# Kernel optimization log

Measured on AMD Instinct MI355X. Metric: run time of the kernel, lower is better.

## Reference

```python
import jax, jax.numpy as jnp
import numpy as np

B, S, D_MODEL, H = 2, 2048, 1024, 16
HD = D_MODEL // H  # head_dim = 64


def _rope_sincos(seq_len, dim, dtype=jnp.float32):
    # inv_freq = 1 / 10000**(arange(0, dim, 2)/dim)
    inv_freq = 1.0 / (10000.0 ** (jnp.arange(0, dim, 2, dtype=dtype) / dim))
    ang = jnp.arange(seq_len, dtype=dtype)[:, None] * inv_freq[None, :]  # [S, dim/2]
    # reshape for broadcast over the head axis of [B, S, H, dim]
    return jnp.sin(ang)[:, None, :], jnp.cos(ang)[:, None, :]  # [S,1,dim/2]


def _apply_rope(x, sin, cos):
    # x: [B, S, H, HD]; interleaved even/odd rotation, matching
    # stack([x1*cos - x2*sin, x1*sin + x2*cos], -1).flatten(-2,-1)
    x1, x2 = x[..., 0::2], x[..., 1::2]
    rot = jnp.stack([x1 * cos - x2 * sin, x1 * sin + x2 * cos], axis=-1)
    return rot.reshape(x.shape)


def setup_inputs() -> dict:
    key = jax.random.key(0)
    ks = jax.random.split(key, 9)
    std = 0.02
    inp = {
        "hidden_states": jax.random.normal(ks[0], (B, S, D_MODEL), jnp.float32),
        "attention_mask": jnp.zeros((1, 1, S, S), jnp.float32),
        "Wq": jax.random.normal(ks[1], (D_MODEL, D_MODEL), jnp.float32) * std,
        "bq": jnp.zeros((D_MODEL,), jnp.float32),
        "Wk": jax.random.normal(ks[2], (D_MODEL, D_MODEL), jnp.float32) * std,
        "bk": jnp.zeros((D_MODEL,), jnp.float32),
        "Wv": jax.random.normal(ks[3], (D_MODEL, D_MODEL), jnp.float32) * std,
        "bv": jnp.zeros((D_MODEL,), jnp.float32),
        "Wo": jax.random.normal(ks[4], (D_MODEL, D_MODEL), jnp.float32) * std,
        "bo": jnp.zeros((D_MODEL,), jnp.float32),
    }
    return inp


def reference(hidden_states, attention_mask, Wq, bq, Wk, bk, Wv, bv, Wo, bo):
    b, s, d = hidden_states.shape
    # QKV projections -> [B, S, H, HD]
    q = (hidden_states @ Wq + bq).reshape(b, s, H, HD)
    k = (hidden_states @ Wk + bk).reshape(b, s, H, HD)
    v = (hidden_states @ Wv + bv).reshape(b, s, H, HD)

    sin, cos = _rope_sincos(s, HD, hidden_states.dtype)
    q = _apply_rope(q, sin, cos)
    k = _apply_rope(k, sin, cos)

    scale = 1.0 / jnp.sqrt(jnp.asarray(HD, hidden_states.dtype))
    # [B, H, S, S]
    scores = jnp.einsum("bqhd,bkhd->bhqk", q, k) * scale + attention_mask
    probs = jax.nn.softmax(scores, axis=-1)
    # [B, S, H, HD] -> [B, S, D]
    ctx = jnp.einsum("bhqk,bkhd->bqhd", probs, v).reshape(b, s, d)
    return ctx @ Wo + bo
```

## Files before the change

kernel.cpp:

```cpp
#include <hip/hip_runtime.h>
#include <hip/hip_bf16.h>

typedef unsigned short u16;
typedef __attribute__((ext_vector_type(8))) __bf16 bf16x8;
typedef __attribute__((ext_vector_type(4))) float f32x4;
typedef __attribute__((ext_vector_type(16))) float f32x16;
typedef __attribute__((ext_vector_type(4))) unsigned uint4v;

#define AS1 __attribute__((address_space(1)))
#define AS3 __attribute__((address_space(3)))

#define S_LEN 2048
#define NH 16
#define DM 1024
#define BATCH 2

__device__ __forceinline__ u16 f2b(float f) {
  union { float f; unsigned u; } v; v.f = f;
  unsigned r = v.u + 0x7FFFu + ((v.u >> 16) & 1u);
  return (u16)(r >> 16);
}

__device__ __forceinline__ unsigned pk2(float lo, float hi) {
  __bf16 l = (__bf16)lo, h = (__bf16)hi;
  unsigned short ul = __builtin_bit_cast(unsigned short, l);
  unsigned short uh = __builtin_bit_cast(unsigned short, h);
  return (unsigned)ul | ((unsigned)uh << 16);
}

__device__ __forceinline__ float exp2_raw(float x) {
  float r;
  asm("v_exp_f32 %0, %1" : "=v"(r) : "v"(x));
  return r;
}

__global__ void rope_table_kernel(float2* __restrict__ t) {
  int idx = blockIdx.x * 256 + threadIdx.x;
  if (idx < S_LEN * 32) {
    int s = idx >> 5, i = idx & 31;
    float inv = powf(10000.f, -(float)i * (1.f / 32.f));
    float ang = (float)s * inv;
    t[idx] = make_float2(sinf(ang), cosf(ang));
  }
}

__global__ void cvt_bf16_kernel(const float* __restrict__ x, u16* __restrict__ y) {
  int i = (blockIdx.x * 256 + threadIdx.x) * 4;
  float4 v = *(const float4*)(x + i);
  *(ushort4*)(y + i) = make_ushort4(f2b(v.x), f2b(v.y), f2b(v.z), f2b(v.w));
}

__global__ void transpose_all_kernel(const float* __restrict__ Wq, const float* __restrict__ Wk,
                                     const float* __restrict__ Wv, const float* __restrict__ Wo,
                                     u16* __restrict__ out) {
  __shared__ float tile[32][33];
  const int z = blockIdx.z;
  const float* W = z == 0 ? Wq : z == 1 ? Wk : z == 2 ? Wv : Wo;
  u16* Wt = out + (size_t)z * DM * DM;
  const int bx = blockIdx.x * 32;
  const int by = blockIdx.y * 32;
  const int tx = threadIdx.x, ty = threadIdx.y;
  for (int i = ty; i < 32; i += 8)
    tile[i][tx] = W[(size_t)(by + i) * DM + bx + tx];
  __syncthreads();
  for (int i = ty; i < 32; i += 8)
    Wt[(size_t)(bx + i) * DM + by + tx] = f2b(tile[tx][i]);
}

template <int MODE>
__global__ __launch_bounds__(256) void gemm128(const u16* __restrict__ A,
                                               const u16* __restrict__ Bt,
                                               const float* __restrict__ bias0,
                                               const float* __restrict__ bias1,
                                               const float* __restrict__ bias2,
                                               void* __restrict__ out0,
                                               void* __restrict__ out1,
                                               void* __restrict__ out2,
                                               const float2* __restrict__ sc,
                                               float escale) {
  __shared__ u16 Al[128 * 32];
  __shared__ u16 Bl[128 * 32];
  const int t = threadIdx.x;
  const int lane = t & 63;
  const int wid = t >> 6;
  const int wr = wid >> 1, wc = wid & 1;
  const int row0 = blockIdx.x * 128, col0 = blockIdx.y * 128;

  const int arow = t >> 2, acol = (t & 3) * 8;
  const u16* gA0 = A + (size_t)(row0 + arow) * DM + acol;
  const u16* gA1 = gA0 + (size_t)64 * DM;
  const u16* gB0 = Bt + (size_t)(col0 + arow) * DM + acol;
  const u16* gB1 = gB0 + (size_t)64 * DM;

  f32x4 acc[4][4] = {};

  for (int k0 = 0; k0 < DM; k0 += 32) {
    __builtin_amdgcn_global_load_lds((const AS1 void*)(gA0 + k0), (AS3 void*)(&Al[t * 8]), 16, 0, 0);
    __builtin_amdgcn_global_load_lds((const AS1 void*)(gA1 + k0), (AS3 void*)(&Al[2048 + t * 8]), 16, 0, 0);
    __builtin_amdgcn_global_load_lds((const AS1 void*)(gB0 + k0), (AS3 void*)(&Bl[t * 8]), 16, 0, 0);
    __builtin_amdgcn_global_load_lds((const AS1 void*)(gB1 + k0), (AS3 void*)(&Bl[2048 + t * 8]), 16, 0, 0);
    __syncthreads();
    bf16x8 af[4], bfr[4];
#pragma unroll
    for (int m = 0; m < 4; ++m)
      af[m] = *(const bf16x8*)&Al[(wr * 64 + m * 16 + (lane & 15)) * 32 + (lane >> 4) * 8];
#pragma unroll
    for (int n = 0; n < 4; ++n)
      bfr[n] = *(const bf16x8*)&Bl[(wc * 64 + n * 16 + (lane & 15)) * 32 + (lane >> 4) * 8];
#pragma unroll
    for (int m = 0; m < 4; ++m)
#pragma unroll
      for (int n = 0; n < 4; ++n)
        acc[m][n] = __builtin_amdgcn_mfma_f32_16x16x32_bf16(af[m], bfr[n], acc[m][n], 0, 0, 0);
    __syncthreads();
  }

  const int sec = (MODE == 3) ? (col0 >> 10) : 0;
  const float* bias = (MODE == 3) ? (sec == 0 ? bias0 : sec == 1 ? bias1 : bias2) : bias0;
  const float es = (MODE == 3 && sec != 0) ? 1.f : escale;

#pragma unroll
  for (int m = 0; m < 4; ++m) {
#pragma unroll
    for (int n = 0; n < 4; ++n) {
      const int col = col0 + wc * 64 + n * 16 + (lane & 15);
      const float bcol = bias[col & 1023];
      const int rbase = row0 + wr * 64 + m * 16 + ((lane >> 4) << 2);
      if constexpr (MODE == 3) {
        const int colr = col & 1023;
        const int h = colr >> 6, d = colr & 63;
        if (sec < 2) {
          u16* O = (u16*)(sec == 0 ? out0 : out1);
          const int ip = d >> 1;
#pragma unroll
          for (int r = 0; r < 4; ++r) {
            const int row = rbase + r;
            const int bb = row >> 11, ss = row & (S_LEN - 1);
            float v = acc[m][n][r] + bcol;
            float pr = __shfl_xor(v, 1, 64);
            float2 scv = sc[ss * 32 + ip];
            float o = (d & 1) ? fmaf(pr, scv.x, v * scv.y) : fmaf(-pr, scv.x, v * scv.y);
            O[((size_t)(bb * NH + h) * S_LEN + ss) * 64 + d] = f2b(o * es);
          }
        } else {
          u16* O = (u16*)out2;
#pragma unroll
          for (int r = 0; r < 4; ++r) {
            const int row = rbase + r;
            const int bb = row >> 11, ss = row & (S_LEN - 1);
            O[((size_t)(bb * NH + h) * 64 + d) * S_LEN + ss] = f2b(acc[m][n][r] + bcol);
          }
        }
      } else {
        float* O = (float*)out0;
#pragma unroll
        for (int r = 0; r < 4; ++r) {
          const int row = rbase + r;
          O[(size_t)row * DM + col] = acc[m][n][r] + bcol;
        }
      }
    }
  }
}

__global__ __launch_bounds__(256, 2) void attn64(const u16* __restrict__ Qa,
                                                 const u16* __restrict__ Ka,
                                                 const u16* __restrict__ Vt,
                                                 u16* __restrict__ Ctx) {
  __shared__ u16 Kl[2][8192];
  __shared__ u16 Vl[2][8192];
  const int t = threadIdx.x, lane = t & 63, w = t >> 6;
  const int l31 = lane & 31, hi = lane >> 5;

  const int wg = blockIdx.x;
  const int swz = (wg & 7) * 64 + (wg >> 3);
  const int bh = swz >> 4, qb = swz & 15;
  const int bb = bh / NH, h = bh % NH;
  const u16* Q = Qa + (size_t)bh * S_LEN * 64;
  const u16* K = Ka + (size_t)bh * S_LEN * 64;
  const u16* V = Vt + (size_t)bh * 64 * S_LEN;
  const int qr0 = qb * 128 + w * 32;

  bf16x8 bQ[4];
#pragma unroll
  for (int kc = 0; kc < 4; ++kc)
    bQ[kc] = *(const bf16x8*)&Q[(size_t)(qr0 + l31) * 64 + kc * 16 + hi * 8];

  int off0[4];
#pragma unroll
  for (int kc = 0; kc < 4; ++kc) {
    const int cb = kc * 32 + hi * 16;
    off0[kc] = l31 * 128 + (cb ^ ((l31 & 7) << 4));
  }

  float mrun = -3.0e38f, lrun = 0.f;
  f32x16 acco0 = {}, acco1 = {};

#define STAGE64(kv, c, hf)                                                               \
  {                                                                                      \
    _Pragma("unroll") for (int is = 0; is < 2; ++is) {                                   \
      const int o = is * 4096 + t * 16;                                                  \
      const int row = o >> 7;                                                            \
      const int cs = (o & 127) ^ ((row & 7) << 4);                                       \
      __builtin_amdgcn_global_load_lds((const AS1 void*)(K + (size_t)((kv) + row) * 64 + (cs >> 1)), \
                                       (AS3 void*)(&Kl[c][(hf) * 4096 + (o >> 1)]), 16, 0, 0); \
      __builtin_amdgcn_global_load_lds((const AS1 void*)(V + (size_t)row * S_LEN + (kv) + (cs >> 1)), \
                                       (AS3 void*)(&Vl[c][(hf) * 4096 + (o >> 1)]), 16, 0, 0); \
    }                                                                                    \
  }
#define STAGE128(kv, c) { STAGE64((kv), c, 0); STAGE64((kv) + 64, c, 1); }

  STAGE128(0, 0);
  __syncthreads();
  int cur = 0;

  for (int it = 0; it < S_LEN / 128; ++it) {
    if (it + 1 < S_LEN / 128) STAGE128((it + 1) * 128, cur ^ 1);

#pragma unroll
    for (int hf = 0; hf < 2; ++hf) {
      const char* KC = (const char*)Kl[cur] + hf * 8192;
      const char* VC = (const char*)Vl[cur] + hf * 8192;

      f32x16 s0 = {}, s1 = {};
      __builtin_amdgcn_s_setprio(1);
#pragma unroll
      for (int kc = 0; kc < 4; ++kc) {
        bf16x8 aK0 = *(const bf16x8*)(KC + off0[kc]);
        bf16x8 aK1 = *(const bf16x8*)(KC + off0[kc] + 4096);
        s0 = __builtin_amdgcn_mfma_f32_32x32x16_bf16(aK0, bQ[kc], s0, 0, 0, 0);
        s1 = __builtin_amdgcn_mfma_f32_32x32x16_bf16(aK1, bQ[kc], s1, 0, 0, 0);
      }
      __builtin_amdgcn_s_setprio(0);

      float p[32];
#pragma unroll
      for (int i = 0; i < 16; ++i) { p[i] = s0[i]; p[16 + i] = s1[i]; }

      float mm[10];
#pragma unroll
      for (int i = 0; i < 10; ++i)
        mm[i] = fmaxf(fmaxf(p[3 * i], p[3 * i + 1]), p[3 * i + 2]);
      const float n0 = fmaxf(fmaxf(mm[0], mm[1]), mm[2]);
      const float n1 = fmaxf(fmaxf(mm[3], mm[4]), mm[5]);
      const float n2 = fmaxf(fmaxf(mm[6], mm[7]), mm[8]);
      const float n3 = fmaxf(mm[9], fmaxf(p[30], p[31]));
      float pmax = fmaxf(fmaxf(n0, n1), fmaxf(n2, n3));
      pmax = fmaxf(pmax, __shfl_xor(pmax, 32, 64));

      if (!__all(pmax - mrun <= 8.f)) {
        const float mnew = fmaxf(mrun, pmax);
        const float al = exp2_raw(mrun - mnew);
#pragma unroll
        for (int i = 0; i < 16; ++i) { acco0[i] *= al; acco1[i] *= al; }
        lrun *= al;
        mrun = mnew;
      }
#pragma unroll
      for (int i = 0; i < 32; ++i) p[i] = exp2_raw(p[i] - mrun);

      float b16[16];
#pragma unroll
      for (int i = 0; i < 16; ++i) b16[i] = p[i] + p[16 + i];
      float b8[8];
#pragma unroll
      for (int i = 0; i < 8; ++i) b8[i] = b16[i] + b16[8 + i];
      float b4[4];
#pragma unroll
      for (int i = 0; i < 4; ++i) b4[i] = b8[i] + b8[4 + i];
      float rs = (b4[0] + b4[1]) + (b4[2] + b4[3]);
      rs += __shfl_xor(rs, 32, 64);
      lrun += rs;

#pragma unroll
      for (int ch = 0; ch < 4; ++ch) {
        const int base = (ch >> 1) * 16 + (ch & 1) * 8;
        unsigned a0 = pk2(p[base + 0], p[base + 1]);
        unsigned b0 = pk2(p[base + 2], p[base + 3]);
        unsigned a8 = pk2(p[base + 4], p[base + 5]);
        unsigned b8w = pk2(p[base + 6], p[base + 7]);
        asm("v_permlane32_swap_b32 %0, %1" : "+v"(a0), "+v"(a8));
        asm("v_permlane32_swap_b32 %0, %1" : "+v"(b0), "+v"(b8w));
        uint4v bw;
        bw[0] = a0; bw[1] = b0; bw[2] = a8; bw[3] = b8w;
        const bf16x8 bP = __builtin_bit_cast(bf16x8, bw);
        bf16x8 aV0 = *(const bf16x8*)(VC + off0[ch]);
        bf16x8 aV1 = *(const bf16x8*)(VC + off0[ch] + 4096);
        __builtin_amdgcn_s_setprio(1);
        acco0 = __builtin_amdgcn_mfma_f32_32x32x16_bf16(aV0, bP, acco0, 0, 0, 0);
        acco1 = __builtin_amdgcn_mfma_f32_32x32x16_bf16(aV1, bP, acco1, 0, 0, 0);
        __builtin_amdgcn_s_setprio(0);
      }
    }

    __syncthreads();
    cur ^= 1;
  }

  const float inv = 1.f / lrun;
  const size_t rowbase = ((size_t)bb * S_LEN + qr0 + l31) * DM + h * 64;
#pragma unroll
  for (int u = 0; u < 4; ++u) {
    ushort4 o0, o1;
    o0.x = f2b(acco0[4 * u + 0] * inv); o0.y = f2b(acco0[4 * u + 1] * inv);
    o0.z = f2b(acco0[4 * u + 2] * inv); o0.w = f2b(acco0[4 * u + 3] * inv);
    o1.x = f2b(acco1[4 * u + 0] * inv); o1.y = f2b(acco1[4 * u + 1] * inv);
    o1.z = f2b(acco1[4 * u + 2] * inv); o1.w = f2b(acco1[4 * u + 3] * inv);
    *(ushort4*)&Ctx[rowbase + 8 * u + 4 * hi] = o0;
    *(ushort4*)&Ctx[rowbase + 32 + 8 * u + 4 * hi] = o1;
  }
}

extern "C" void kernel_launch(void* const* d_in, const int* in_sizes, int n_in,
                              void* d_out, int out_size, void* d_ws, size_t ws_size,
                              hipStream_t stream) {
  const float* hs = (const float*)d_in[0];
  const float* Wq = (const float*)d_in[2];
  const float* bq = (const float*)d_in[3];
  const float* Wk = (const float*)d_in[4];
  const float* bk = (const float*)d_in[5];
  const float* Wv = (const float*)d_in[6];
  const float* bv = (const float*)d_in[7];
  const float* Wo = (const float*)d_in[8];
  const float* bo = (const float*)d_in[9];

  u16* Xbf = (u16*)d_ws;
  u16* Wt4 = Xbf + (size_t)4096 * 1024;
  u16* Qa  = Wt4 + (size_t)4096 * 1024;
  u16* Ka  = Qa + (size_t)4096 * 1024;
  u16* Vtb = Ka + (size_t)4096 * 1024;
  u16* Ctx = Vtb + (size_t)4096 * 1024;
  float2* scT = (float2*)(Ctx + (size_t)4096 * 1024);

  const float SC = 0.125f * 1.44269504088896f;

  rope_table_kernel<<<dim3(256), dim3(256), 0, stream>>>(scT);
  cvt_bf16_kernel<<<dim3(4096), dim3(256), 0, stream>>>(hs, Xbf);
  transpose_all_kernel<<<dim3(32, 32, 4), dim3(32, 8), 0, stream>>>(Wq, Wk, Wv, Wo, Wt4);

  gemm128<3><<<dim3(32, 24), dim3(256), 0, stream>>>(Xbf, Wt4, bq, bk, bv,
                                                     (void*)Qa, (void*)Ka, (void*)Vtb, scT, SC);

  attn64<<<dim3(512), dim3(256), 0, stream>>>(Qa, Ka, Vtb, Ctx);

  gemm128<2><<<dim3(32, 8), dim3(256), 0, stream>>>(Ctx, Wt4 + (size_t)3 * DM * DM, bo,
                                                    nullptr, nullptr, d_out, nullptr, nullptr,
                                                    nullptr, 1.f);
}
```

Before: 147.3 us.

## Split attention KV across waves, merge prep kernels, narrow output GEMM tiles

Three preprocessing kernels are merged into one launch to cut launch overhead. The attention kernel now processes 64 query rows per block with two wave pairs each covering half of the key/value sequence, combining partial softmax states through LDS at the end. It drops double-buffered prefetch in favour of higher occupancy (4 blocks/SM) and twice the blocks. The output projection uses 128x64 tiles to double its grid for better CU fill, at the cost of more A-matrix reloads.

New measurement: 139.3 us. 1.06x faster.

```diff
diff --git a/kernel.cpp b/kernel.cpp
--- a/kernel.cpp
+++ b/kernel.cpp
@@ -34,50 +34,51 @@
   return r;
 }
 
-__global__ void rope_table_kernel(float2* __restrict__ t) {
-  int idx = blockIdx.x * 256 + threadIdx.x;
-  if (idx < S_LEN * 32) {
-    int s = idx >> 5, i = idx & 31;
+__global__ __launch_bounds__(256) void prep_kernel(const float* __restrict__ hs,
+                                                   const float* __restrict__ Wq,
+                                                   const float* __restrict__ Wk,
+                                                   const float* __restrict__ Wv,
+                                                   const float* __restrict__ Wo,
+                                                   u16* __restrict__ Xbf,
+                                                   u16* __restrict__ Wt4,
+                                                   float2* __restrict__ scT) {
+  __shared__ float tile[32][33];
+  const int bid = blockIdx.x, t = threadIdx.x;
+  if (bid < 4096) {
+    const int i = (bid * 256 + t) * 4;
+    float4 v = *(const float4*)(hs + i);
+    *(ushort4*)(Xbf + i) = make_ushort4(f2b(v.x), f2b(v.y), f2b(v.z), f2b(v.w));
+  } else if (bid < 8192) {
+    const int zb = bid - 4096;
+    const int z = zb >> 10, rem = zb & 1023;
+    const int bx = (rem & 31) * 32, by = (rem >> 5) * 32;
+    const float* W = z == 0 ? Wq : z == 1 ? Wk : z == 2 ? Wv : Wo;
+    u16* Wt = Wt4 + (size_t)z * DM * DM;
+    const int tx = t & 31, ty = t >> 5;
+    for (int i = ty; i < 32; i += 8)
+      tile[i][tx] = W[(size_t)(by + i) * DM + bx + tx];
+    __syncthreads();
+    for (int i = ty; i < 32; i += 8)
+      Wt[(size_t)(bx + i) * DM + by + tx] = f2b(tile[tx][i]);
+  } else {
+    const int idx = (bid - 8192) * 256 + t;
+    const int s = idx >> 5, i = idx & 31;
     float inv = powf(10000.f, -(float)i * (1.f / 32.f));
     float ang = (float)s * inv;
-    t[idx] = make_float2(sinf(ang), cosf(ang));
-  }
-}
-
-__global__ void cvt_bf16_kernel(const float* __restrict__ x, u16* __restrict__ y) {
-  int i = (blockIdx.x * 256 + threadIdx.x) * 4;
-  float4 v = *(const float4*)(x + i);
-  *(ushort4*)(y + i) = make_ushort4(f2b(v.x), f2b(v.y), f2b(v.z), f2b(v.w));
-}
-
-__global__ void transpose_all_kernel(const float* __restrict__ Wq, const float* __restrict__ Wk,
-                                     const float* __restrict__ Wv, const float* __restrict__ Wo,
-                                     u16* __restrict__ out) {
-  __shared__ float tile[32][33];
-  const int z = blockIdx.z;
-  const float* W = z == 0 ? Wq : z == 1 ? Wk : z == 2 ? Wv : Wo;
-  u16* Wt = out + (size_t)z * DM * DM;
-  const int bx = blockIdx.x * 32;
-  const int by = blockIdx.y * 32;
-  const int tx = threadIdx.x, ty = threadIdx.y;
-  for (int i = ty; i < 32; i += 8)
-    tile[i][tx] = W[(size_t)(by + i) * DM + bx + tx];
-  __syncthreads();
-  for (int i = ty; i < 32; i += 8)
-    Wt[(size_t)(bx + i) * DM + by + tx] = f2b(tile[tx][i]);
-}
-
-template <int MODE>
-__global__ __launch_bounds__(256) void gemm128(const u16* __restrict__ A,
-                                               const u16* __restrict__ Bt,
-                                               const float* __restrict__ bias0,
-                                               const float* __restrict__ bias1,
-                                               const float* __restrict__ bias2,
-                                               void* __restrict__ out0,
-                                               void* __restrict__ out1,
-                                               void* __restrict__ out2,
-                                               const float2* __restrict__ sc,
-                                               float escale) {
+    scT[idx] = make_float2(sinf(ang), cosf(ang));
+  }
+}
+
+__global__ __launch_bounds__(256) void gemm_qkv(const u16* __restrict__ A,
+                                                const u16* __restrict__ Bt,
+                                                const float* __restrict__ bias0,
+                                                const float* __restrict__ bias1,
+                                                const float* __restrict__ bias2,
+                                                u16* __restrict__ out0,
+                                                u16* __restrict__ out1,
+                                                u16* __restrict__ out2,
+                                                const float2* __restrict__ sc,
+                                                float escale) {
   __shared__ u16 Al[128 * 32];
   __shared__ u16 Bl[128 * 32];
   const int t = threadIdx.x;
@@ -115,9 +116,9 @@
     __syncthreads();
   }
 
-  const int sec = (MODE == 3) ? (col0 >> 10) : 0;
-  const float* bias = (MODE == 3) ? (sec == 0 ? bias0 : sec == 1 ? bias1 : bias2) : bias0;
-  const float es = (MODE == 3 && sec != 0) ? 1.f : escale;
+  const int sec = col0 >> 10;
+  const float* bias = sec == 0 ? bias0 : sec == 1 ? bias1 : bias2;
+  const float es = sec == 0 ? escale : 1.f;
 
 #pragma unroll
   for (int m = 0; m < 4; ++m) {
@@ -126,60 +127,106 @@
       const int col = col0 + wc * 64 + n * 16 + (lane & 15);
       const float bcol = bias[col & 1023];
       const int rbase = row0 + wr * 64 + m * 16 + ((lane >> 4) << 2);
-      if constexpr (MODE == 3) {
-        const int colr = col & 1023;
-        const int h = colr >> 6, d = colr & 63;
-        if (sec < 2) {
-          u16* O = (u16*)(sec == 0 ? out0 : out1);
-          const int ip = d >> 1;
-#pragma unroll
-          for (int r = 0; r < 4; ++r) {
-            const int row = rbase + r;
-            const int bb = row >> 11, ss = row & (S_LEN - 1);
-            float v = acc[m][n][r] + bcol;
-            float pr = __shfl_xor(v, 1, 64);
-            float2 scv = sc[ss * 32 + ip];
-            float o = (d & 1) ? fmaf(pr, scv.x, v * scv.y) : fmaf(-pr, scv.x, v * scv.y);
-            O[((size_t)(bb * NH + h) * S_LEN + ss) * 64 + d] = f2b(o * es);
-          }
-        } else {
-          u16* O = (u16*)out2;
-#pragma unroll
-          for (int r = 0; r < 4; ++r) {
-            const int row = rbase + r;
-            const int bb = row >> 11, ss = row & (S_LEN - 1);
-            O[((size_t)(bb * NH + h) * 64 + d) * S_LEN + ss] = f2b(acc[m][n][r] + bcol);
-          }
+      const int colr = col & 1023;
+      const int h = colr >> 6, d = colr & 63;
+      if (sec < 2) {
+        u16* O = sec == 0 ? out0 : out1;
+        const int ip = d >> 1;
+#pragma unroll
+        for (int r = 0; r < 4; ++r) {
+          const int row = rbase + r;
+          const int bb = row >> 11, ss = row & (S_LEN - 1);
+          float v = acc[m][n][r] + bcol;
+          float pr = __shfl_xor(v, 1, 64);
+          float2 scv = sc[ss * 32 + ip];
+          float o = (d & 1) ? fmaf(pr, scv.x, v * scv.y) : fmaf(-pr, scv.x, v * scv.y);
+          O[((size_t)(bb * NH + h) * S_LEN + ss) * 64 + d] = f2b(o * es);
         }
       } else {
-        float* O = (float*)out0;
+        u16* O = out2;
 #pragma unroll
         for (int r = 0; r < 4; ++r) {
           const int row = rbase + r;
-          O[(size_t)row * DM + col] = acc[m][n][r] + bcol;
+          const int bb = row >> 11, ss = row & (S_LEN - 1);
+          O[((size_t)(bb * NH + h) * 64 + d) * S_LEN + ss] = f2b(acc[m][n][r] + bcol);
         }
       }
     }
   }
 }
 
-__global__ __launch_bounds__(256, 2) void attn64(const u16* __restrict__ Qa,
+__global__ __launch_bounds__(256) void gemm_o(const u16* __restrict__ A,
+                                              const u16* __restrict__ Bt,
+                                              const float* __restrict__ bias,
+                                              float* __restrict__ O) {
+  __shared__ u16 Al[128 * 32];
+  __shared__ u16 Bl[64 * 32];
+  const int t = threadIdx.x;
+  const int lane = t & 63;
+  const int wid = t >> 6;
+  const int wr = wid >> 1, wc = wid & 1;
+  const int row0 = blockIdx.x * 128, col0 = blockIdx.y * 64;
+
+  const int arow = t >> 2, acol = (t & 3) * 8;
+  const u16* gA0 = A + (size_t)(row0 + arow) * DM + acol;
+  const u16* gA1 = gA0 + (size_t)64 * DM;
+  const u16* gB0 = Bt + (size_t)(col0 + arow) * DM + acol;
+
+  f32x4 acc[4][2] = {};
+
+  for (int k0 = 0; k0 < DM; k0 += 32) {
+    __builtin_amdgcn_global_load_lds((const AS1 void*)(gA0 + k0), (AS3 void*)(&Al[t * 8]), 16, 0, 0);
+    __builtin_amdgcn_global_load_lds((const AS1 void*)(gA1 + k0), (AS3 void*)(&Al[2048 + t * 8]), 16, 0, 0);
+    __builtin_amdgcn_global_load_lds((const AS1 void*)(gB0 + k0), (AS3 void*)(&Bl[t * 8]), 16, 0, 0);
+    __syncthreads();
+    bf16x8 af[4], bfr[2];
+#pragma unroll
+    for (int m = 0; m < 4; ++m)
+      af[m] = *(const bf16x8*)&Al[(wr * 64 + m * 16 + (lane & 15)) * 32 + (lane >> 4) * 8];
+#pragma unroll
+    for (int n = 0; n < 2; ++n)
+      bfr[n] = *(const bf16x8*)&Bl[(wc * 32 + n * 16 + (lane & 15)) * 32 + (lane >> 4) * 8];
+#pragma unroll
+    for (int m = 0; m < 4; ++m)
+#pragma unroll
+      for (int n = 0; n < 2; ++n)
+        acc[m][n] = __builtin_amdgcn_mfma_f32_16x16x32_bf16(af[m], bfr[n], acc[m][n], 0, 0, 0);
+    __syncthreads();
+  }
+
+#pragma unroll
+  for (int m = 0; m < 4; ++m) {
+#pragma unroll
+    for (int n = 0; n < 2; ++n) {
+      const int col = col0 + wc * 32 + n * 16 + (lane & 15);
+      const float bcol = bias[col];
+      const int rbase = row0 + wr * 64 + m * 16 + ((lane >> 4) << 2);
+#pragma unroll
+      for (int r = 0; r < 4; ++r)
+        O[(size_t)(rbase + r) * DM + col] = acc[m][n][r] + bcol;
+    }
+  }
+}
+
+__global__ __launch_bounds__(256, 4) void attn64(const u16* __restrict__ Qa,
                                                  const u16* __restrict__ Ka,
                                                  const u16* __restrict__ Vt,
                                                  u16* __restrict__ Ctx) {
-  __shared__ u16 Kl[2][8192];
-  __shared__ u16 Vl[2][8192];
+  __shared__ u16 KVl[4][4096];
+  __shared__ float Lm[4][64], Ll[4][64];
   const int t = threadIdx.x, lane = t & 63, w = t >> 6;
   const int l31 = lane & 31, hi = lane >> 5;
+  const int qg = w >> 1, ks = w & 1;
 
   const int wg = blockIdx.x;
-  const int swz = (wg & 7) * 64 + (wg >> 3);
-  const int bh = swz >> 4, qb = swz & 15;
+  const int swz = (wg & 7) * 128 + (wg >> 3);
+  const int bh = swz >> 5, qb = swz & 31;
   const int bb = bh / NH, h = bh % NH;
   const u16* Q = Qa + (size_t)bh * S_LEN * 64;
   const u16* K = Ka + (size_t)bh * S_LEN * 64;
   const u16* V = Vt + (size_t)bh * 64 * S_LEN;
-  const int qr0 = qb * 128 + w * 32;
+  const int qr0 = qb * 64 + qg * 32;
+  const int kvb = ks * 1024;
 
   bf16x8 bQ[4];
 #pragma unroll
@@ -196,118 +243,134 @@
   float mrun = -3.0e38f, lrun = 0.f;
   f32x16 acco0 = {}, acco1 = {};
 
-#define STAGE64(kv, c, hf)                                                               \
-  {                                                                                      \
-    _Pragma("unroll") for (int is = 0; is < 2; ++is) {                                   \
-      const int o = is * 4096 + t * 16;                                                  \
-      const int row = o >> 7;                                                            \
-      const int cs = (o & 127) ^ ((row & 7) << 4);                                       \
-      __builtin_amdgcn_global_load_lds((const AS1 void*)(K + (size_t)((kv) + row) * 64 + (cs >> 1)), \
-                                       (AS3 void*)(&Kl[c][(hf) * 4096 + (o >> 1)]), 16, 0, 0); \
-      __builtin_amdgcn_global_load_lds((const AS1 void*)(V + (size_t)row * S_LEN + (kv) + (cs >> 1)), \
-                                       (AS3 void*)(&Vl[c][(hf) * 4096 + (o >> 1)]), 16, 0, 0); \
-    }                                                                                    \
-  }
-#define STAGE128(kv, c) { STAGE64((kv), c, 0); STAGE64((kv) + 64, c, 1); }
-
-  STAGE128(0, 0);
+  for (int it = 0; it < 16; ++it) {
+#pragma unroll
+    for (int is = 0; is < 2; ++is) {
+      const int o = is * 4096 + t * 16;
+      const int row = o >> 7;
+      const int cs = (o & 127) ^ ((row & 7) << 4);
+      const int kv0 = it * 64;
+      __builtin_amdgcn_global_load_lds((const AS1 void*)(K + (size_t)(kv0 + row) * 64 + (cs >> 1)),
+                                       (AS3 void*)(&KVl[0][o >> 1]), 16, 0, 0);
+      __builtin_amdgcn_global_load_lds((const AS1 void*)(K + (size_t)(1024 + kv0 + row) * 64 + (cs >> 1)),
+                                       (AS3 void*)(&KVl[1][o >> 1]), 16, 0, 0);
+      __builtin_amdgcn_global_load_lds((const AS1 void*)(V + (size_t)row * S_LEN + kv0 + (cs >> 1)),
+                                       (AS3 void*)(&KVl[2][o >> 1]), 16, 0, 0);
+      __builtin_amdgcn_global_load_lds((const AS1 void*)(V + (size_t)row * S_LEN + 1024 + kv0 + (cs >> 1)),
+                                       (AS3 void*)(&KVl[3][o >> 1]), 16, 0, 0);
+    }
+    __syncthreads();
+
+    const char* KC = (const char*)KVl[ks];
+    const char* VC = (const char*)KVl[2 + ks];
+
+    f32x16 s0 = {}, s1 = {};
+    __builtin_amdgcn_s_setprio(1);
+#pragma unroll
+    for (int kc = 0; kc < 4; ++kc) {
+      bf16x8 aK0 = *(const bf16x8*)(KC + off0[kc]);
+      bf16x8 aK1 = *(const bf16x8*)(KC + off0[kc] + 4096);
+      s0 = __builtin_amdgcn_mfma_f32_32x32x16_bf16(aK0, bQ[kc], s0, 0, 0, 0);
+      s1 = __builtin_amdgcn_mfma_f32_32x32x16_bf16(aK1, bQ[kc], s1, 0, 0, 0);
+    }
+    __builtin_amdgcn_s_setprio(0);
+
+    float p[32];
+#pragma unroll
+    for (int i = 0; i < 16; ++i) { p[i] = s0[i]; p[16 + i] = s1[i]; }
+
+    float mm[10];
+#pragma unroll
+    for (int i = 0; i < 10; ++i)
+      mm[i] = fmaxf(fmaxf(p[3 * i], p[3 * i + 1]), p[3 * i + 2]);
+    const float n0 = fmaxf(fmaxf(mm[0], mm[1]), mm[2]);
+    const float n1 = fmaxf(fmaxf(mm[3], mm[4]), mm[5]);
+    const float n2 = fmaxf(fmaxf(mm[6], mm[7]), mm[8]);
+    const float n3 = fmaxf(mm[9], fmaxf(p[30], p[31]));
+    float pmax = fmaxf(fmaxf(n0, n1), fmaxf(n2, n3));
+    pmax = fmaxf(pmax, __shfl_xor(pmax, 32, 64));
+
+    if (!__all(pmax - mrun <= 8.f)) {
+      const float mnew = fmaxf(mrun, pmax);
+      const float al = exp2_raw(mrun - mnew);
+#pragma unroll
+      for (int i = 0; i < 16; ++i) { acco0[i] *= al; acco1[i] *= al; }
+      lrun *= al;
+      mrun = mnew;
+    }
+#pragma unroll
+    for (int i = 0; i < 32; ++i) p[i] = exp2_raw(p[i] - mrun);
+
+    float b16[16];
+#pragma unroll
+    for (int i = 0; i < 16; ++i) b16[i] = p[i] + p[16 + i];
+    float b8[8];
+#pragma unroll
+    for (int i = 0; i < 8; ++i) b8[i] = b16[i] + b16[8 + i];
+    float b4[4];
+#pragma unroll
+    for (int i = 0; i < 4; ++i) b4[i] = b8[i] + b8[4 + i];
+    float rs = (b4[0] + b4[1]) + (b4[2] + b4[3]);
+    rs += __shfl_xor(rs, 32, 64);
+    lrun += rs;
+
+#pragma unroll
+    for (int ch = 0; ch < 4; ++ch) {
+      const int base = (ch >> 1) * 16 + (ch & 1) * 8;
+      unsigned a0 = pk2(p[base + 0], p[base + 1]);
+      unsigned b0 = pk2(p[base + 2], p[base + 3]);
+      unsigned a8 = pk2(p[base + 4], p[base + 5]);
+      unsigned b8w = pk2(p[base + 6], p[base + 7]);
+      asm("v_permlane32_swap_b32 %0, %1" : "+v"(a0), "+v"(a8));
+      asm("v_permlane32_swap_b32 %0, %1" : "+v"(b0), "+v"(b8w));
+      uint4v bw;
+      bw[0] = a0; bw[1] = b0; bw[2] = a8; bw[3] = b8w;
+      const bf16x8 bP = __builtin_bit_cast(bf16x8, bw);
+      bf16x8 aV0 = *(const bf16x8*)(VC + off0[ch]);
+      bf16x8 aV1 = *(const bf16x8*)(VC + off0[ch] + 4096);
+      __builtin_amdgcn_s_setprio(1);
+      acco0 = __builtin_amdgcn_mfma_f32_32x32x16_bf16(aV0, bP, acco0, 0, 0, 0);
+      acco1 = __builtin_amdgcn_mfma_f32_32x32x16_bf16(aV1, bP, acco1, 0, 0, 0);
+      __builtin_amdgcn_s_setprio(0);
+    }
+
+    __syncthreads();
+  }
+
+  Lm[w][lane] = mrun;
+  Ll[w][lane] = lrun;
   __syncthreads();
-  int cur = 0;
-
-  for (int it = 0; it < S_LEN / 128; ++it) {
-    if (it + 1 < S_LEN / 128) STAGE128((it + 1) * 128, cur ^ 1);
-
-#pragma unroll
-    for (int hf = 0; hf < 2; ++hf) {
-      const char* KC = (const char*)Kl[cur] + hf * 8192;
-      const char* VC = (const char*)Vl[cur] + hf * 8192;
-
-      f32x16 s0 = {}, s1 = {};
-      __builtin_amdgcn_s_setprio(1);
-#pragma unroll
-      for (int kc = 0; kc < 4; ++kc) {
-        bf16x8 aK0 = *(const bf16x8*)(KC + off0[kc]);
-        bf16x8 aK1 = *(const bf16x8*)(KC + off0[kc] + 4096);
-        s0 = __builtin_amdgcn_mfma_f32_32x32x16_bf16(aK0, bQ[kc], s0, 0, 0, 0);
-        s1 = __builtin_amdgcn_mfma_f32_32x32x16_bf16(aK1, bQ[kc], s1, 0, 0, 0);
-      }
-      __builtin_amdgcn_s_setprio(0);
-
-      float p[32];
-#pragma unroll
-      for (int i = 0; i < 16; ++i) { p[i] = s0[i]; p[16 + i] = s1[i]; }
-
-      float mm[10];
-#pragma unroll
-      for (int i = 0; i < 10; ++i)
-        mm[i] = fmaxf(fmaxf(p[3 * i], p[3 * i + 1]), p[3 * i + 2]);
-      const float n0 = fmaxf(fmaxf(mm[0], mm[1]), mm[2]);
-      const float n1 = fmaxf(fmaxf(mm[3], mm[4]), mm[5]);
-      const float n2 = fmaxf(fmaxf(mm[6], mm[7]), mm[8]);
-      const float n3 = fmaxf(mm[9], fmaxf(p[30], p[31]));
-      float pmax = fmaxf(fmaxf(n0, n1), fmaxf(n2, n3));
-      pmax = fmaxf(pmax, __shfl_xor(pmax, 32, 64));
-
-      if (!__all(pmax - mrun <= 8.f)) {
-        const float mnew = fmaxf(mrun, pmax);
-        const float al = exp2_raw(mrun - mnew);
-#pragma unroll
-        for (int i = 0; i < 16; ++i) { acco0[i] *= al; acco1[i] *= al; }
-        lrun *= al;
-        mrun = mnew;
-      }
-#pragma unroll
-      for (int i = 0; i < 32; ++i) p[i] = exp2_raw(p[i] - mrun);
-
-      float b16[16];
-#pragma unroll
-      for (int i = 0; i < 16; ++i) b16[i] = p[i] + p[16 + i];
-      float b8[8];
-#pragma unroll
-      for (int i = 0; i < 8; ++i) b8[i] = b16[i] + b16[8 + i];
-      float b4[4];
-#pragma unroll
-      for (int i = 0; i < 4; ++i) b4[i] = b8[i] + b8[4 + i];
-      float rs = (b4[0] + b4[1]) + (b4[2] + b4[3]);
-      rs += __shfl_xor(rs, 32, 64);
-      lrun += rs;
-
-#pragma unroll
-      for (int ch = 0; ch < 4; ++ch) {
-        const int base = (ch >> 1) * 16 + (ch & 1) * 8;
-        unsigned a0 = pk2(p[base + 0], p[base + 1]);
-        unsigned b0 = pk2(p[base + 2], p[base + 3]);
-        unsigned a8 = pk2(p[base + 4], p[base + 5]);
-        unsigned b8w = pk2(p[base + 6], p[base + 7]);
-        asm("v_permlane32_swap_b32 %0, %1" : "+v"(a0), "+v"(a8));
-        asm("v_permlane32_swap_b32 %0, %1" : "+v"(b0), "+v"(b8w));
-        uint4v bw;
-        bw[0] = a0; bw[1] = b0; bw[2] = a8; bw[3] = b8w;
-        const bf16x8 bP = __builtin_bit_cast(bf16x8, bw);
-        bf16x8 aV0 = *(const bf16x8*)(VC + off0[ch]);
-        bf16x8 aV1 = *(const bf16x8*)(VC + off0[ch] + 4096);
-        __builtin_amdgcn_s_setprio(1);
-        acco0 = __builtin_amdgcn_mfma_f32_32x32x16_bf16(aV0, bP, acco0, 0, 0, 0);
-        acco1 = __builtin_amdgcn_mfma_f32_32x32x16_bf16(aV1, bP, acco1, 0, 0, 0);
-        __builtin_amdgcn_s_setprio(0);
-      }
-    }
-
-    __syncthreads();
-    cur ^= 1;
-  }
-
-  const float inv = 1.f / lrun;
-  const size_t rowbase = ((size_t)bb * S_LEN + qr0 + l31) * DM + h * 64;
-#pragma unroll
-  for (int u = 0; u < 4; ++u) {
-    ushort4 o0, o1;
-    o0.x = f2b(acco0[4 * u + 0] * inv); o0.y = f2b(acco0[4 * u + 1] * inv);
-    o0.z = f2b(acco0[4 * u + 2] * inv); o0.w = f2b(acco0[4 * u + 3] * inv);
-    o1.x = f2b(acco1[4 * u + 0] * inv); o1.y = f2b(acco1[4 * u + 1] * inv);
-    o1.z = f2b(acco1[4 * u + 2] * inv); o1.w = f2b(acco1[4 * u + 3] * inv);
-    *(ushort4*)&Ctx[rowbase + 8 * u + 4 * hi] = o0;
-    *(ushort4*)&Ctx[rowbase + 32 + 8 * u + 4 * hi] = o1;
+  const float m_p = Lm[w ^ 1][lane], l_p = Ll[w ^ 1][lane];
+  const float mf = fmaxf(mrun, m_p);
+  const float a_s = exp2_raw(mrun - mf);
+  const float a_p = exp2_raw(m_p - mf);
+  const float lf = lrun * a_s + l_p * a_p;
+
+  float* Ob = (float*)&KVl[0][0];
+  if (ks == 1) {
+    float* dst = Ob + (qg * 64 + lane) * 36;
+#pragma unroll
+    for (int i = 0; i < 16; ++i) { dst[i] = acco0[i] * a_s; dst[16 + i] = acco1[i] * a_s; }
+  }
+  __syncthreads();
+  if (ks == 0) {
+    const float* src = Ob + (qg * 64 + lane) * 36;
+    const float inv = 1.f / lf;
+    const size_t rowbase = ((size_t)bb * S_LEN + qr0 + l31) * DM + h * 64;
+#pragma unroll
+    for (int u = 0; u < 4; ++u) {
+      ushort4 o0, o1;
+      o0.x = f2b((acco0[4 * u + 0] * a_s + src[4 * u + 0]) * inv);
+      o0.y = f2b((acco0[4 * u + 1] * a_s + src[4 * u + 1]) * inv);
+      o0.z = f2b((acco0[4 * u + 2] * a_s + src[4 * u + 2]) * inv);
+      o0.w = f2b((acco0[4 * u + 3] * a_s + src[4 * u + 3]) * inv);
+      o1.x = f2b((acco1[4 * u + 0] * a_s + src[16 + 4 * u + 0]) * inv);
+      o1.y = f2b((acco1[4 * u + 1] * a_s + src[16 + 4 * u + 1]) * inv);
+      o1.z = f2b((acco1[4 * u + 2] * a_s + src[16 + 4 * u + 2]) * inv);
+      o1.w = f2b((acco1[4 * u + 3] * a_s + src[16 + 4 * u + 3]) * inv);
+      *(ushort4*)&Ctx[rowbase + 8 * u + 4 * hi] = o0;
+      *(ushort4*)&Ctx[rowbase + 32 + 8 * u + 4 * hi] = o1;
+    }
   }
 }
 
@@ -334,16 +397,13 @@
 
   const float SC = 0.125f * 1.44269504088896f;
 
-  rope_table_kernel<<<dim3(256), dim3(256), 0, stream>>>(scT);
-  cvt_bf16_kernel<<<dim3(4096), dim3(256), 0, stream>>>(hs, Xbf);
-  transpose_all_kernel<<<dim3(32, 32, 4), dim3(32, 8), 0, stream>>>(Wq, Wk, Wv, Wo, Wt4);
-
-  gemm128<3><<<dim3(32, 24), dim3(256), 0, stream>>>(Xbf, Wt4, bq, bk, bv,
-                                                     (void*)Qa, (void*)Ka, (void*)Vtb, scT, SC);
-
-  attn64<<<dim3(512), dim3(256), 0, stream>>>(Qa, Ka, Vtb, Ctx);
-
-  gemm128<2><<<dim3(32, 8), dim3(256), 0, stream>>>(Ctx, Wt4 + (size_t)3 * DM * DM, bo,
-                                                    nullptr, nullptr, d_out, nullptr, nullptr,
-                                                    nullptr, 1.f);
-}
+  prep_kernel<<<dim3(8448), dim3(256), 0, stream>>>(hs, Wq, Wk, Wv, Wo, Xbf, Wt4, scT);
+
+  gemm_qkv<<<dim3(32, 24), dim3(256), 0, stream>>>(Xbf, Wt4, bq, bk, bv,
+                                                   Qa, Ka, Vtb, scT, SC);
+
+  attn64<<<dim3(1024), dim3(256), 0, stream>>>(Qa, Ka, Vtb, Ctx);
+
+  gemm_o<<<dim3(32, 16), dim3(256), 0, stream>>>(Ctx, Wt4 + (size_t)3 * DM * DM, bo,
+                                                 (float*)d_out);
+}
```
